# Optimization experiments

Measured on AMD Instinct MI355X. Metric: run time of the kernel, lower is better.

Reference implementation:

```python
import jax, jax.numpy as jnp
from jax import lax
import numpy as np

CH = 16      # channel_n
HID = 128    # update MLP width


def setup_inputs() -> dict:
    key = jax.random.key(0)
    ks = jax.random.split(key, 7)
    B, H, W = 4, 224, 224
    x = jax.random.uniform(ks[0], (B, CH, H, W), dtype=jnp.float32)
    # perception: Conv2d(16 -> 48, 3x3, pad 1, no bias), OIHW
    w_percep = jax.random.normal(ks[1], (CH * 3, CH, 3, 3), jnp.float32) * 0.05
    # update MLP: 1x1 convs == pointwise linears over channels
    w1 = jax.random.normal(ks[2], (HID, CH * 3), jnp.float32) * 0.05
    b1 = jax.random.normal(ks[3], (HID,), jnp.float32) * 0.01
    w2 = jax.random.normal(ks[4], (HID, HID), jnp.float32) * 0.05
    b2 = jax.random.normal(ks[5], (HID,), jnp.float32) * 0.01
    w3 = jax.random.normal(ks[6], (CH, HID), jnp.float32) * 0.05  # no bias
    return {"x": x, "w_percep": w_percep, "w1": w1, "b1": b1,
            "w2": w2, "b2": b2, "w3": w3, "steps": 40}


def reference(x, w_percep, w1, b1, w2, b2, w3, steps):
    dn = ("NCHW", "OIHW", "NCHW")

    def step(x, _):
        # 3x3 perception conv, same padding  -> [B, 48, H, W]
        p = lax.conv_general_dilated(x, w_percep, (1, 1), "SAME",
                                     dimension_numbers=dn)
        # pointwise conv-MLP (1x1 convs as channel einsums)
        h = jax.nn.relu(jnp.einsum("bchw,oc->bohw", p, w1) + b1[None, :, None, None])
        h = jax.nn.relu(jnp.einsum("bchw,oc->bohw", h, w2) + b2[None, :, None, None])
        dx = jnp.einsum("bchw,oc->bohw", h, w3)
        # residual update + clamp to [0, 1] (eval mode: no fire mask)
        return jnp.clip(x + dx, 0.0, 1.0), None

    x, _ = lax.scan(step, x, None, length=steps)
    return x
```

## Files before the change

### kernel.cpp

```cpp
#include <hip/hip_runtime.h>


typedef __attribute__((ext_vector_type(8))) short short8;
typedef __attribute__((ext_vector_type(4))) float float4v;
typedef __attribute__((ext_vector_type(2))) float float2v;

#define MFMA16(a, b, c) __builtin_amdgcn_mfma_f32_16x16x32_bf16((a), (b), (c), 0, 0, 0)

__device__ __forceinline__ short f2bf(float f) {
  unsigned u = __builtin_bit_cast(unsigned, f);
  return (short)((u + 0x8000u) >> 16);
}

__device__ __forceinline__ unsigned pk2bf(float a, float b) {
#if __has_builtin(__builtin_amdgcn_cvt_pk_bf16_f32)
  typedef __attribute__((ext_vector_type(2))) __bf16 bf2;
  bf2 r = __builtin_amdgcn_cvt_pk_bf16_f32(a, b);
  return __builtin_bit_cast(unsigned, r);
#else
  unsigned ua = __builtin_bit_cast(unsigned, a), ub = __builtin_bit_cast(unsigned, b);
  return ((ua + 0x8000u) >> 16) | (((ub + 0x8000u) >> 16) << 16);
#endif
}

__device__ __forceinline__ void async16(const void* g, void* l) {
  __builtin_amdgcn_global_load_lds((const __attribute__((address_space(1))) void*)g,
                                   (__attribute__((address_space(3))) void*)l,
                                   16, 0, 0);
}

__device__ __forceinline__ void sync_lds() {
  asm volatile("s_waitcnt lgkmcnt(0)\n\ts_barrier" ::: "memory");
}

#define WS_WE    0
#define WS_W2    43008
#define WS_W3    77824
#define WS_B1    82944
#define WS_B2    83456
#define WS_X32A  83968
#define WS_X32B  12929024
#define WS_X16A  25774080
#define WS_X16B  32196608

__global__ void prep_x(const float* __restrict__ x, float* __restrict__ x32,
                       short* __restrict__ x16) {
  int i = blockIdx.x * 256 + threadIdx.x;
  int w = i % 224;
  int h = (i / 224) % 224;
  int c = (i / 50176) & 15;
  int bb = i / 802816;
  float v = x[i];
  int o = ((bb * 224 + h) * 224 + w) * 16 + c;
  x32[o] = v;
  x16[o] = f2bf(v);
}

__global__ void prep_w(const float* __restrict__ wp, const float* __restrict__ w1,
                       const float* __restrict__ b1, const float* __restrict__ w2,
                       const float* __restrict__ b2, const float* __restrict__ w3,
                       short* __restrict__ wE, short* __restrict__ w2t,
                       short* __restrict__ w3t, float* __restrict__ b1p,
                       float* __restrict__ b2p) {
  int i = blockIdx.x * 256 + threadIdx.x;
  if (i < 21504) {
    int o = i / 168, k = i % 168;
    float v = 0.f;
    if (k < 144) {
      int off = k >> 4, c = k & 15;
      for (int c3 = 0; c3 < 48; ++c3)
        v += w1[o * 48 + c3] * wp[c3 * 144 + c * 9 + off];
    }
    wE[i] = f2bf(v);
  } else if (i < 38912) {
    int j = i - 21504;
    int n = j / 136, kk = j % 136;
    float v = 0.f;
    if (kk < 128) { int ch = 16 * (kk & 7) + (kk >> 3); v = w2[n * 128 + ch]; }
    w2t[j] = f2bf(v);
  } else if (i < 41472) {
    int j = i - 38912;
    float v = 0.f;
    if (j < 2176) {
      int n = j / 136, kk = j % 136;
      if (kk < 128) { int ch = 16 * (kk & 7) + (kk >> 3); v = w3[n * 128 + ch]; }
    }
    w3t[j] = f2bf(v);
  } else if (i < 41600) {
    int p = i - 41472;
    b1p[p] = b1[16 * (p & 7) + (p >> 3)];
  } else {
    int p = i - 41600;
    b2p[p] = b2[16 * (p & 7) + (p >> 3)];
  }
}

template <bool LAST>
__global__ __launch_bounds__(512, 4) void ca_step(
    const short* __restrict__ wEg, const short* __restrict__ w2g,
    const short* __restrict__ w3g, const float* __restrict__ b1p,
    const float* __restrict__ b2p, const float* __restrict__ xs32,
    const short* __restrict__ xs16, float* __restrict__ xd32,
    short* __restrict__ xd16, float* __restrict__ dout) {
  __shared__ short sXH[4 * 3616];
  __shared__ short sBUF[2 * 2 * 2176];
  __shared__ short sH2[2 * 2 * 2176];

  const int tid = threadIdx.x;
  const int lane = tid & 63;
  const int wv = tid >> 6;
  const int c16 = lane & 15;
  const int q = lane >> 4;
  const int q8 = q * 8;
  const int qh = q >> 1;
  const int c0 = (q & 1) * 8;

  const int blk = blockIdx.x;
  const int b = blk / 112;
  const int h0 = (blk % 112) * 2;

  const short8 z8 = {0, 0, 0, 0, 0, 0, 0, 0};
  for (int t = wv; t < 28; t += 8) {
    int hr = t / 7, ck = t % 7;
    int hh = h0 - 1 + hr;
    char* l = (char*)sXH + hr * 7232 + 32 + ck * 1024;
    if (hh >= 0 && hh < 224) {
      const char* g = (const char*)xs16 + ((size_t)(b * 224 + hh) * 224) * 32 + ck * 1024;
      async16(g + lane * 16, l);
    } else {
      *(short8*)(l + lane * 16) = z8;
    }
  }
  if (tid < 16) {
    int hr = tid >> 2, wch = tid & 3;
    int colb = (wch < 2) ? 0 : 225;
    *(short8*)((char*)sXH + hr * 7232 + colb * 32 + (wch & 1) * 16) = z8;
  }

  if (wv < 4) {
    const int wq = wv;
    short8 wf[5][2];
#pragma unroll
    for (int kc = 0; kc < 5; ++kc)
#pragma unroll
      for (int n = 0; n < 2; ++n)
        wf[kc][n] = *(const short8*)(wEg + ((2 * wq + n) * 16 + c16) * 168 + kc * 32 + q8);
    const float2v bH = *(const float2v*)(b1p + c16 * 8 + 2 * wq);

    __syncthreads();

    for (int j = 0; j < 16; ++j) {
      if (j < 14) {
        const int t0 = 2 * j, t1 = t0 + 1;
        const int hb0 = ((t0 / 14) * 226 + (t0 % 14) * 16) * 16;
        const int hb1 = ((t1 / 14) * 226 + (t1 % 14) * 16) * 16;
        float4v acc[2][2];
#pragma unroll
        for (int tt = 0; tt < 2; ++tt)
#pragma unroll
          for (int n = 0; n < 2; ++n) acc[tt][n] = (float4v){0.f, 0.f, 0.f, 0.f};
#pragma unroll
        for (int kc = 0; kc < 5; ++kc) {
          int off = kc * 2 + qh;
          if (off > 8) off = 8;
          int dy = (off * 11) >> 5;
          int dxx = off - dy * 3;
          const int ao = (dy * 226 + dxx + c16) * 16 + c0;
          short8 a0 = *(const short8*)(sXH + hb0 + ao);
          short8 a1 = *(const short8*)(sXH + hb1 + ao);
#pragma unroll
          for (int n = 0; n < 2; ++n) {
            acc[0][n] = MFMA16(a0, wf[kc][n], acc[0][n]);
            acc[1][n] = MFMA16(a1, wf[kc][n], acc[1][n]);
          }
        }
#pragma unroll
        for (int tt = 0; tt < 2; ++tt) {
          short* dst = sBUF + ((j & 1) * 2 + tt) * 2176;
#pragma unroll
          for (int r = 0; r < 4; ++r) {
            unsigned d = pk2bf(fmaxf(acc[tt][0][r] + bH[0], 0.f),
                               fmaxf(acc[tt][1][r] + bH[1], 0.f));
            *(unsigned*)(dst + (q * 4 + r) * 136 + c16 * 8 + 2 * wq) = d;
          }
        }
      }
      sync_lds();
    }
  } else {
    const int g = wv - 4;
    short8 w2f[4][2];
    short8 w3f[4];
#pragma unroll
    for (int kc = 0; kc < 4; ++kc)
#pragma unroll
      for (int n = 0; n < 2; ++n)
        w2f[kc][n] = *(const short8*)(w2g + ((2 * g + n) * 16 + c16) * 136 + kc * 32 + q8);
#pragma unroll
    for (int kc = 0; kc < 4; ++kc)
      w3f[kc] = *(const short8*)(w3g + c16 * 136 + kc * 32 + q8);
    const float2v bG = *(const float2v*)(b2p + c16 * 8 + 2 * g);

    __syncthreads();

    for (int j = 0; j < 16; ++j) {
      float xres[4];
      int cb3 = 0, hglob3 = 0;
      if (g < 2 && j >= 2) {
        const int t3 = 2 * (j - 2) + g;
        cb3 = (t3 % 14) * 16; hglob3 = h0 + t3 / 14;
#pragma unroll
        for (int r = 0; r < 4; ++r) {
          size_t pix = (size_t)(b * 224 + hglob3) * 224 + cb3 + q * 4 + r;
          xres[r] = xs32[pix * 16 + c16];
        }
      }
      if (j >= 1 && j <= 14) {
        const short* srcA = sBUF + (((j - 1) & 1) * 2 + 0) * 2176;
        const short* srcB = sBUF + (((j - 1) & 1) * 2 + 1) * 2176;
        float4v acc2[2][2];
#pragma unroll
        for (int tt = 0; tt < 2; ++tt)
#pragma unroll
          for (int n = 0; n < 2; ++n) acc2[tt][n] = (float4v){0.f, 0.f, 0.f, 0.f};
#pragma unroll
        for (int kc = 0; kc < 4; ++kc) {
          short8 aA = *(const short8*)(srcA + c16 * 136 + kc * 32 + q8);
          short8 aB = *(const short8*)(srcB + c16 * 136 + kc * 32 + q8);
#pragma unroll
          for (int n = 0; n < 2; ++n) {
            acc2[0][n] = MFMA16(aA, w2f[kc][n], acc2[0][n]);
            acc2[1][n] = MFMA16(aB, w2f[kc][n], acc2[1][n]);
          }
        }
#pragma unroll
        for (int tt = 0; tt < 2; ++tt) {
          short* dsth2 = sH2 + ((j & 1) * 2 + tt) * 2176;
#pragma unroll
          for (int r = 0; r < 4; ++r) {
            unsigned d = pk2bf(fmaxf(acc2[tt][0][r] + bG[0], 0.f),
                               fmaxf(acc2[tt][1][r] + bG[1], 0.f));
            *(unsigned*)(dsth2 + (q * 4 + r) * 136 + c16 * 8 + 2 * g) = d;
          }
        }
      }
      if (g < 2 && j >= 2) {
        const short* srch2 = sH2 + (((j - 1) & 1) * 2 + g) * 2176;
        float4v acc3 = (float4v){0.f, 0.f, 0.f, 0.f};
#pragma unroll
        for (int kc = 0; kc < 4; ++kc) {
          short8 a = *(const short8*)(srch2 + c16 * 136 + kc * 32 + q8);
          acc3 = MFMA16(a, w3f[kc], acc3);
        }
#pragma unroll
        for (int r = 0; r < 4; ++r) {
          int col = cb3 + q * 4 + r;
          size_t pix = (size_t)(b * 224 + hglob3) * 224 + col;
          float v = xres[r] + acc3[r];
          v = fminf(fmaxf(v, 0.f), 1.f);
          if (LAST) {
            dout[((size_t)(b * 16 + c16) * 224 + hglob3) * 224 + col] = v;
          } else {
            xd32[pix * 16 + c16] = v;
            xd16[pix * 16 + c16] = f2bf(v);
          }
        }
      }
      sync_lds();
    }
  }
}

extern "C" void kernel_launch(void* const* d_in, const int* in_sizes, int n_in,
                              void* d_out, int out_size, void* d_ws, size_t ws_size,
                              hipStream_t stream) {
  const float* x  = (const float*)d_in[0];
  const float* wp = (const float*)d_in[1];
  const float* w1 = (const float*)d_in[2];
  const float* b1 = (const float*)d_in[3];
  const float* w2 = (const float*)d_in[4];
  const float* b2 = (const float*)d_in[5];
  const float* w3 = (const float*)d_in[6];

  char* ws = (char*)d_ws;
  short* wEg = (short*)(ws + WS_WE);
  short* w2g = (short*)(ws + WS_W2);
  short* w3g = (short*)(ws + WS_W3);
  float* b1p = (float*)(ws + WS_B1);
  float* b2p = (float*)(ws + WS_B2);
  float* X32[2] = {(float*)(ws + WS_X32A), (float*)(ws + WS_X32B)};
  short* X16[2] = {(short*)(ws + WS_X16A), (short*)(ws + WS_X16B)};

  prep_x<<<12544, 256, 0, stream>>>(x, X32[0], X16[0]);
  prep_w<<<163, 256, 0, stream>>>(wp, w1, b1, w2, b2, w3, wEg, w2g, w3g, b1p, b2p);

  for (int s = 0; s < 39; ++s) {
    int sb = s & 1;
    ca_step<false><<<448, 512, 0, stream>>>(wEg, w2g, w3g, b1p, b2p,
                                            X32[sb], X16[sb],
                                            X32[1 - sb], X16[1 - sb], nullptr);
  }
  ca_step<true><<<448, 512, 0, stream>>>(wEg, w2g, w3g, b1p, b2p,
                                         X32[1], X16[1],
                                         X32[0], X16[0], (float*)d_out);
}
```

Measured before the change: 1.004 ms.

## Repartition MLP waves to own one tile and four output fragments

```diff
diff --git a/kernel.cpp b/kernel.cpp
--- a/kernel.cpp
+++ b/kernel.cpp
@@ -4,6 +4,7 @@
 typedef __attribute__((ext_vector_type(8))) short short8;
 typedef __attribute__((ext_vector_type(4))) float float4v;
 typedef __attribute__((ext_vector_type(2))) float float2v;
+typedef __attribute__((ext_vector_type(2))) unsigned int uint2v;
 
 #define MFMA16(a, b, c) __builtin_amdgcn_mfma_f32_16x16x32_bf16((a), (b), (c), 0, 0, 0)
 
@@ -138,115 +139,101 @@
   }
 
   if (wv < 4) {
-    const int wq = wv;
-    short8 wf[5][2];
+    const int half = wv & 1;
+    const int tt = wv >> 1;
+    short8 wf[5][4];
 #pragma unroll
     for (int kc = 0; kc < 5; ++kc)
 #pragma unroll
-      for (int n = 0; n < 2; ++n)
-        wf[kc][n] = *(const short8*)(wEg + ((2 * wq + n) * 16 + c16) * 168 + kc * 32 + q8);
-    const float2v bH = *(const float2v*)(b1p + c16 * 8 + 2 * wq);
+      for (int nf = 0; nf < 4; ++nf)
+        wf[kc][nf] = *(const short8*)(wEg + ((4 * half + nf) * 16 + c16) * 168 + kc * 32 + q8);
+    const float4v bH = *(const float4v*)(b1p + c16 * 8 + half * 4);
 
     __syncthreads();
 
     for (int j = 0; j < 16; ++j) {
       if (j < 14) {
-        const int t0 = 2 * j, t1 = t0 + 1;
-        const int hb0 = ((t0 / 14) * 226 + (t0 % 14) * 16) * 16;
-        const int hb1 = ((t1 / 14) * 226 + (t1 % 14) * 16) * 16;
-        float4v acc[2][2];
-#pragma unroll
-        for (int tt = 0; tt < 2; ++tt)
-#pragma unroll
-          for (int n = 0; n < 2; ++n) acc[tt][n] = (float4v){0.f, 0.f, 0.f, 0.f};
+        const int t = 2 * j + tt;
+        const int hb = ((t / 14) * 226 + (t % 14) * 16) * 16;
+        float4v acc[4];
+#pragma unroll
+        for (int nf = 0; nf < 4; ++nf) acc[nf] = (float4v){0.f, 0.f, 0.f, 0.f};
 #pragma unroll
         for (int kc = 0; kc < 5; ++kc) {
           int off = kc * 2 + qh;
           if (off > 8) off = 8;
           int dy = (off * 11) >> 5;
           int dxx = off - dy * 3;
-          const int ao = (dy * 226 + dxx + c16) * 16 + c0;
-          short8 a0 = *(const short8*)(sXH + hb0 + ao);
-          short8 a1 = *(const short8*)(sXH + hb1 + ao);
-#pragma unroll
-          for (int n = 0; n < 2; ++n) {
-            acc[0][n] = MFMA16(a0, wf[kc][n], acc[0][n]);
-            acc[1][n] = MFMA16(a1, wf[kc][n], acc[1][n]);
-          }
-        }
-#pragma unroll
-        for (int tt = 0; tt < 2; ++tt) {
-          short* dst = sBUF + ((j & 1) * 2 + tt) * 2176;
-#pragma unroll
-          for (int r = 0; r < 4; ++r) {
-            unsigned d = pk2bf(fmaxf(acc[tt][0][r] + bH[0], 0.f),
-                               fmaxf(acc[tt][1][r] + bH[1], 0.f));
-            *(unsigned*)(dst + (q * 4 + r) * 136 + c16 * 8 + 2 * wq) = d;
-          }
+          short8 a = *(const short8*)(sXH + hb + (dy * 226 + dxx + c16) * 16 + c0);
+#pragma unroll
+          for (int nf = 0; nf < 4; ++nf) acc[nf] = MFMA16(a, wf[kc][nf], acc[nf]);
+        }
+        short* dst = sBUF + ((j & 1) * 2 + tt) * 2176;
+#pragma unroll
+        for (int r = 0; r < 4; ++r) {
+          unsigned d0 = pk2bf(fmaxf(acc[0][r] + bH[0], 0.f),
+                              fmaxf(acc[1][r] + bH[1], 0.f));
+          unsigned d1 = pk2bf(fmaxf(acc[2][r] + bH[2], 0.f),
+                              fmaxf(acc[3][r] + bH[3], 0.f));
+          *(uint2v*)(dst + (q * 4 + r) * 136 + c16 * 8 + half * 4) = (uint2v){d0, d1};
         }
       }
       sync_lds();
     }
   } else {
-    const int g = wv - 4;
-    short8 w2f[4][2];
+    const int v = wv - 4;
+    const int half = v & 1;
+    const int tt = v >> 1;
+    short8 w2f[4][4];
+#pragma unroll
+    for (int kc = 0; kc < 4; ++kc)
+#pragma unroll
+      for (int nf = 0; nf < 4; ++nf)
+        w2f[kc][nf] = *(const short8*)(w2g + ((4 * half + nf) * 16 + c16) * 136 + kc * 32 + q8);
     short8 w3f[4];
-#pragma unroll
-    for (int kc = 0; kc < 4; ++kc)
-#pragma unroll
-      for (int n = 0; n < 2; ++n)
-        w2f[kc][n] = *(const short8*)(w2g + ((2 * g + n) * 16 + c16) * 136 + kc * 32 + q8);
 #pragma unroll
     for (int kc = 0; kc < 4; ++kc)
       w3f[kc] = *(const short8*)(w3g + c16 * 136 + kc * 32 + q8);
-    const float2v bG = *(const float2v*)(b2p + c16 * 8 + 2 * g);
+    const float4v bG = *(const float4v*)(b2p + c16 * 8 + half * 4);
 
     __syncthreads();
 
     for (int j = 0; j < 16; ++j) {
-      float xres[4];
+      float4v acc3;
       int cb3 = 0, hglob3 = 0;
-      if (g < 2 && j >= 2) {
-        const int t3 = 2 * (j - 2) + g;
+      const bool doG3 = (half == 0) && (j >= 2);
+      if (doG3) {
+        const int t3 = 2 * (j - 2) + tt;
         cb3 = (t3 % 14) * 16; hglob3 = h0 + t3 / 14;
 #pragma unroll
         for (int r = 0; r < 4; ++r) {
           size_t pix = (size_t)(b * 224 + hglob3) * 224 + cb3 + q * 4 + r;
-          xres[r] = xs32[pix * 16 + c16];
+          acc3[r] = xs32[pix * 16 + c16];
         }
       }
       if (j >= 1 && j <= 14) {
-        const short* srcA = sBUF + (((j - 1) & 1) * 2 + 0) * 2176;
-        const short* srcB = sBUF + (((j - 1) & 1) * 2 + 1) * 2176;
-        float4v acc2[2][2];
-#pragma unroll
-        for (int tt = 0; tt < 2; ++tt)
-#pragma unroll
-          for (int n = 0; n < 2; ++n) acc2[tt][n] = (float4v){0.f, 0.f, 0.f, 0.f};
+        const short* src = sBUF + (((j - 1) & 1) * 2 + tt) * 2176;
+        float4v acc2[4];
+#pragma unroll
+        for (int nf = 0; nf < 4; ++nf) acc2[nf] = (float4v){0.f, 0.f, 0.f, 0.f};
 #pragma unroll
         for (int kc = 0; kc < 4; ++kc) {
-          short8 aA = *(const short8*)(srcA + c16 * 136 + kc * 32 + q8);
-          short8 aB = *(const short8*)(srcB + c16 * 136 + kc * 32 + q8);
-#pragma unroll
-          for (int n = 0; n < 2; ++n) {
-            acc2[0][n] = MFMA16(aA, w2f[kc][n], acc2[0][n]);
-            acc2[1][n] = MFMA16(aB, w2f[kc][n], acc2[1][n]);
-          }
-        }
-#pragma unroll
-        for (int tt = 0; tt < 2; ++tt) {
-          short* dsth2 = sH2 + ((j & 1) * 2 + tt) * 2176;
-#pragma unroll
-          for (int r = 0; r < 4; ++r) {
-            unsigned d = pk2bf(fmaxf(acc2[tt][0][r] + bG[0], 0.f),
-                               fmaxf(acc2[tt][1][r] + bG[1], 0.f));
-            *(unsigned*)(dsth2 + (q * 4 + r) * 136 + c16 * 8 + 2 * g) = d;
-          }
-        }
-      }
-      if (g < 2 && j >= 2) {
-        const short* srch2 = sH2 + (((j - 1) & 1) * 2 + g) * 2176;
-        float4v acc3 = (float4v){0.f, 0.f, 0.f, 0.f};
+          short8 a = *(const short8*)(src + c16 * 136 + kc * 32 + q8);
+#pragma unroll
+          for (int nf = 0; nf < 4; ++nf) acc2[nf] = MFMA16(a, w2f[kc][nf], acc2[nf]);
+        }
+        short* dsth2 = sH2 + ((j & 1) * 2 + tt) * 2176;
+#pragma unroll
+        for (int r = 0; r < 4; ++r) {
+          unsigned d0 = pk2bf(fmaxf(acc2[0][r] + bG[0], 0.f),
+                              fmaxf(acc2[1][r] + bG[1], 0.f));
+          unsigned d1 = pk2bf(fmaxf(acc2[2][r] + bG[2], 0.f),
+                              fmaxf(acc2[3][r] + bG[3], 0.f));
+          *(uint2v*)(dsth2 + (q * 4 + r) * 136 + c16 * 8 + half * 4) = (uint2v){d0, d1};
+        }
+      }
+      if (doG3) {
+        const short* srch2 = sH2 + (((j - 1) & 1) * 2 + tt) * 2176;
 #pragma unroll
         for (int kc = 0; kc < 4; ++kc) {
           short8 a = *(const short8*)(srch2 + c16 * 136 + kc * 32 + q8);
@@ -256,13 +243,12 @@
         for (int r = 0; r < 4; ++r) {
           int col = cb3 + q * 4 + r;
           size_t pix = (size_t)(b * 224 + hglob3) * 224 + col;
-          float v = xres[r] + acc3[r];
-          v = fminf(fmaxf(v, 0.f), 1.f);
+          float vv = fminf(fmaxf(acc3[r], 0.f), 1.f);
           if (LAST) {
-            dout[((size_t)(b * 16 + c16) * 224 + hglob3) * 224 + col] = v;
+            dout[((size_t)(b * 16 + c16) * 224 + hglob3) * 224 + col] = vv;
           } else {
-            xd32[pix * 16 + c16] = v;
-            xd16[pix * 16 + c16] = f2bf(v);
+            xd32[pix * 16 + c16] = vv;
+            xd16[pix * 16 + c16] = f2bf(vv);
           }
         }
       }
```

Result: slower. 1.045 ms (+4.1%).
